# Optimization experiments

Measured on AMD Instinct MI355X. Metric: run time of the kernel, lower is better.

## Reference

```python
import jax, jax.numpy as jnp
import numpy as np

HEADS = 16

def setup_inputs() -> dict:
    key = jax.random.key(0)
    k1, k2, k3, k4 = jax.random.split(key, 4)
    B, T, S, W = 2, 2048, 2048, 1024
    x = jax.random.normal(k1, (B, T, W), dtype=jnp.float32)
    cond_k = jax.random.normal(k2, (B, S, W), dtype=jnp.float32)
    cond_v = jax.random.normal(k3, (B, S, W), dtype=jnp.float32)
    w_proj = jax.random.normal(k4, (W, W), dtype=jnp.float32) * 0.02
    b_proj = jnp.zeros((W,), dtype=jnp.float32)
    return {"x": x, "cond_k": cond_k, "cond_v": cond_v, "w_proj": w_proj, "b_proj": b_proj}

def reference(x, cond_k, cond_v, w_proj, b_proj):
    B, T, W = x.shape
    S = cond_k.shape[1]
    H = HEADS
    d = W // H
    scale = 1.0 / jnp.sqrt(jnp.sqrt(jnp.float32(d)))  # applied to both q and k
    q = x.reshape(B, T, H, d) * scale
    k = cond_k.reshape(B, S, H, d) * scale
    v = cond_v.reshape(B, S, H, d)
    # scores: [B, H, T, S]
    scores = jnp.einsum('bthd,bshd->bhts', q, k)
    w = jax.nn.softmax(scores.astype(jnp.float32), axis=-1).astype(scores.dtype)
    out = jnp.einsum('bhts,bshd->bthd', w, v).reshape(B, T, W)
    # c_proj: torch Linear -> x @ W.T + b
    return out @ w_proj.T + b_proj
```

## Files before the change

kernel.cpp:

```cpp
#include <hip/hip_runtime.h>

#define Bn 2
#define Hn 16
#define Tn 2048
#define Sn 2048
#define Wd 1024
#define Dh 64

typedef __attribute__((ext_vector_type(8))) short s16x8;
typedef __attribute__((ext_vector_type(4))) short s16x4;
typedef __attribute__((ext_vector_type(4))) float f32x4;

#define MFMA(a, b, c) __builtin_amdgcn_mfma_f32_16x16x32_bf16((a), (b), (c), 0, 0, 0)

__device__ __forceinline__ s16x8 ld8(const short* p) { return *(const s16x8*)p; }

__device__ __forceinline__ short f2bf(float f) {
    unsigned u = __builtin_bit_cast(unsigned, f);
    u += 0x7FFFu + ((u >> 16) & 1u);
    return (short)(u >> 16);
}

__global__ void cvt_scale(const float* __restrict__ in, short* __restrict__ out,
                          int n, float s) {
    int i = (blockIdx.x * 256 + threadIdx.x) * 8;
    if (i < n) {
        float4 a = *(const float4*)(in + i);
        float4 b = *(const float4*)(in + i + 4);
        s16x8 o;
        o[0] = f2bf(a.x * s); o[1] = f2bf(a.y * s); o[2] = f2bf(a.z * s); o[3] = f2bf(a.w * s);
        o[4] = f2bf(b.x * s); o[5] = f2bf(b.y * s); o[6] = f2bf(b.z * s); o[7] = f2bf(b.w * s);
        *(s16x8*)(out + i) = o;
    }
}

__global__ __launch_bounds__(256) void vtrans(const float* __restrict__ cv,
                                              short* __restrict__ vt) {
    __shared__ short T[64][68];
    const int st = blockIdx.x & 31;
    const int bh = blockIdx.x >> 5;
    const int b = bh >> 4, h = bh & 15;
    const int tid = threadIdx.x;
#pragma unroll
    for (int i = 0; i < 4; ++i) {
        int f = i * 256 + tid, sr = f >> 4, c4 = f & 15;
        float4 v = *(const float4*)(cv + (size_t)(b * Sn + st * 64 + sr) * Wd + h * Dh + c4 * 4);
        s16x4 o;
        o[0] = f2bf(v.x); o[1] = f2bf(v.y); o[2] = f2bf(v.z); o[3] = f2bf(v.w);
        *(s16x4*)&T[sr][c4 * 4] = o;
    }
    __syncthreads();
#pragma unroll
    for (int i = 0; i < 4; ++i) {
        int f = i * 256 + tid, dr = f >> 4, p4 = f & 15;
        s16x4 o;
#pragma unroll
        for (int k = 0; k < 4; ++k) {
            int p = p4 * 4 + k;
            int g = p >> 5, pi = p & 31;
            int sl = g * 32 + ((pi & 1) * 16 + (pi >> 1));
            o[k] = T[sl][dr];
        }
        *(s16x4*)(vt + (size_t)(bh * Dh + dr) * Sn + st * 64 + p4 * 4) = o;
    }
}

#define KSTR 72

__global__ __launch_bounds__(256, 2) void attn_fused(
    const float* __restrict__ x, const short* __restrict__ kb,
    const short* __restrict__ vt, short* __restrict__ ao)
{
    __shared__ short Ks[64 * KSTR];
    __shared__ short Vs[64 * KSTR];
    __shared__ short Pt[4][32 * KSTR];

    const int tid  = threadIdx.x;
    const int w    = tid >> 6;
    const int l    = tid & 63;
    const int quad = l >> 4;
    const int l16  = l & 15;

    const int bh = blockIdx.x & 31;
    const int qt = blockIdx.x >> 5;
    const int b  = bh >> 4, h = bh & 15;

    const int qrow0 = qt * 128 + w * 32;

    const float SQ = 0.125f * 1.4426950408889634f;
    s16x8 aq[2][2];
#pragma unroll
    for (int mi = 0; mi < 2; ++mi)
#pragma unroll
        for (int c = 0; c < 2; ++c) {
            const float* p = x + (size_t)(b * Tn + qrow0 + mi * 16 + l16) * Wd
                               + h * Dh + c * 32 + quad * 8;
            float4 a = ((const float4*)p)[0], bb = ((const float4*)p)[1];
            s16x8 o;
            o[0] = f2bf(a.x * SQ); o[1] = f2bf(a.y * SQ); o[2] = f2bf(a.z * SQ); o[3] = f2bf(a.w * SQ);
            o[4] = f2bf(bb.x * SQ); o[5] = f2bf(bb.y * SQ); o[6] = f2bf(bb.z * SQ); o[7] = f2bf(bb.w * SQ);
            aq[mi][c] = o;
        }

    f32x4 oacc[2][4];
    float dn[2][4];
#pragma unroll
    for (int mi = 0; mi < 2; ++mi) {
#pragma unroll
        for (int nt = 0; nt < 4; ++nt) {
            oacc[mi][nt][0] = 0.f; oacc[mi][nt][1] = 0.f;
            oacc[mi][nt][2] = 0.f; oacc[mi][nt][3] = 0.f;
        }
#pragma unroll
        for (int r = 0; r < 4; ++r) dn[mi][r] = 0.f;
    }

    const short* kb_h = kb + (size_t)(b * Sn) * Wd + h * Dh;
    const short* vt_h = vt + (size_t)(bh * Dh) * Sn;

    const int sr = tid >> 3;
    const int sg = tid & 7;

    short* Pw = &Pt[w][0];

    for (int it = 0; it < Sn / 64; ++it) {
        const int s0 = it * 64;
        __syncthreads();
#pragma unroll
        for (int i = 0; i < 2; ++i) {
            int r0 = sr + i * 32;
            *(s16x8*)&Ks[r0 * KSTR + sg * 8] = ld8(kb_h + (size_t)(s0 + r0) * Wd + sg * 8);
            *(s16x8*)&Vs[r0 * KSTR + sg * 8] = ld8(vt_h + (size_t)r0 * Sn + s0 + sg * 8);
        }
        __syncthreads();

        f32x4 sc[2][4];
        const f32x4 z = {0.f, 0.f, 0.f, 0.f};
#pragma unroll
        for (int sj = 0; sj < 4; ++sj) {
            s16x8 k0 = *(const s16x8*)&Ks[(sj * 16 + l16) * KSTR + quad * 8];
            s16x8 k1 = *(const s16x8*)&Ks[(sj * 16 + l16) * KSTR + 32 + quad * 8];
#pragma unroll
            for (int mi = 0; mi < 2; ++mi) {
                sc[mi][sj] = MFMA(aq[mi][0], k0, z);
                sc[mi][sj] = MFMA(aq[mi][1], k1, sc[mi][sj]);
            }
        }

#pragma unroll
        for (int mi = 0; mi < 2; ++mi)
#pragma unroll
            for (int g = 0; g < 2; ++g)
#pragma unroll
                for (int r = 0; r < 4; ++r) {
                    unsigned u0 = __builtin_bit_cast(unsigned, __builtin_amdgcn_exp2f(sc[mi][2 * g][r]));
                    unsigned u1 = __builtin_bit_cast(unsigned, __builtin_amdgcn_exp2f(sc[mi][2 * g + 1][r]));
                    unsigned hi = u1 & 0xFFFF0000u;
                    unsigned pk = (u0 >> 16) | hi;
                    dn[mi][r] += __builtin_bit_cast(float, u0 & 0xFFFF0000u)
                               + __builtin_bit_cast(float, hi);
                    *(unsigned*)&Pw[(mi * 16 + quad * 4 + r) * KSTR + g * 32 + l16 * 2] = pk;
                }
        __asm__ __volatile__("" ::: "memory");

        s16x8 ap[2][2], bv[4][2];
#pragma unroll
        for (int mi = 0; mi < 2; ++mi)
#pragma unroll
            for (int g = 0; g < 2; ++g)
                ap[mi][g] = *(const s16x8*)&Pw[(mi * 16 + l16) * KSTR + g * 32 + quad * 8];
#pragma unroll
        for (int nt = 0; nt < 4; ++nt)
#pragma unroll
            for (int g = 0; g < 2; ++g)
                bv[nt][g] = *(const s16x8*)&Vs[(nt * 16 + l16) * KSTR + g * 32 + quad * 8];
#pragma unroll
        for (int mi = 0; mi < 2; ++mi)
#pragma unroll
            for (int nt = 0; nt < 4; ++nt) {
                oacc[mi][nt] = MFMA(ap[mi][0], bv[nt][0], oacc[mi][nt]);
                oacc[mi][nt] = MFMA(ap[mi][1], bv[nt][1], oacc[mi][nt]);
            }
    }

#pragma unroll
    for (int mi = 0; mi < 2; ++mi)
#pragma unroll
        for (int r = 0; r < 4; ++r) {
            float d = dn[mi][r];
            d += __shfl_xor(d, 1);
            d += __shfl_xor(d, 2);
            d += __shfl_xor(d, 4);
            d += __shfl_xor(d, 8);
            float inv = 1.0f / d;
            int t = qrow0 + mi * 16 + quad * 4 + r;
#pragma unroll
            for (int nt = 0; nt < 4; ++nt)
                ao[(size_t)(b * Tn + t) * Wd + h * Dh + nt * 16 + l16] =
                    f2bf(oacc[mi][nt][r] * inv);
        }
}

#define LSTR 40

__global__ __launch_bounds__(256, 2) void proj_gemm(
    const short* __restrict__ A, const short* __restrict__ Wb,
    const float* __restrict__ bias, float* __restrict__ out)
{
    __shared__ short As[128 * LSTR];
    __shared__ short Bs[64 * LSTR];

    const int tid  = threadIdx.x;
    const int w    = tid >> 6;
    const int l    = tid & 63;
    const int quad = l >> 4;
    const int l16  = l & 15;

    const int bn = blockIdx.x & 15;
    const int bm = blockIdx.x >> 4;
    const int m0 = bm * 128;
    const int n0 = bn * 64;
    const int wm = (w & 1) * 64;
    const int wn = (w >> 1) * 32;

    const int rr = tid >> 2;
    const int sg = tid & 3;

    f32x4 acc[4][2];
#pragma unroll
    for (int mi = 0; mi < 4; ++mi)
#pragma unroll
        for (int nt = 0; nt < 2; ++nt) {
            acc[mi][nt][0] = 0.f; acc[mi][nt][1] = 0.f;
            acc[mi][nt][2] = 0.f; acc[mi][nt][3] = 0.f;
        }

    for (int k0 = 0; k0 < Wd; k0 += 32) {
        __syncthreads();
        *(s16x8*)&As[rr * LSTR + sg * 8]        = ld8(A  + (size_t)(m0 + rr) * Wd + k0 + sg * 8);
        *(s16x8*)&As[(rr + 64) * LSTR + sg * 8] = ld8(A  + (size_t)(m0 + 64 + rr) * Wd + k0 + sg * 8);
        *(s16x8*)&Bs[rr * LSTR + sg * 8]        = ld8(Wb + (size_t)(n0 + rr) * Wd + k0 + sg * 8);
        __syncthreads();

        s16x8 a[4], bw[2];
#pragma unroll
        for (int mi = 0; mi < 4; ++mi)
            a[mi] = *(const s16x8*)&As[(wm + mi * 16 + l16) * LSTR + quad * 8];
#pragma unroll
        for (int nt = 0; nt < 2; ++nt)
            bw[nt] = *(const s16x8*)&Bs[(wn + nt * 16 + l16) * LSTR + quad * 8];
#pragma unroll
        for (int mi = 0; mi < 4; ++mi)
#pragma unroll
            for (int nt = 0; nt < 2; ++nt)
                acc[mi][nt] = MFMA(a[mi], bw[nt], acc[mi][nt]);
    }

#pragma unroll
    for (int nt = 0; nt < 2; ++nt) {
        float bv = bias[n0 + wn + nt * 16 + l16];
#pragma unroll
        for (int mi = 0; mi < 4; ++mi)
#pragma unroll
            for (int r = 0; r < 4; ++r)
                out[(size_t)(m0 + wm + mi * 16 + quad * 4 + r) * Wd + n0 + wn + nt * 16 + l16] =
                    acc[mi][nt][r] + bv;
    }
}

extern "C" void kernel_launch(void* const* d_in, const int* in_sizes, int n_in,
                              void* d_out, int out_size, void* d_ws, size_t ws_size,
                              hipStream_t stream) {
    const float* x  = (const float*)d_in[0];
    const float* ck = (const float*)d_in[1];
    const float* cv = (const float*)d_in[2];
    const float* wp = (const float*)d_in[3];
    const float* bp = (const float*)d_in[4];

    const int nX = Bn * Tn * Wd;
    const int nW = Wd * Wd;

    short* kbb = (short*)d_ws;
    short* vtb = kbb + nX;
    short* wbb = vtb + nX;
    short* am  = wbb + nW;

    cvt_scale<<<dim3(nX / 2048), dim3(256), 0, stream>>>(ck, kbb, nX, 1.0f);
    cvt_scale<<<dim3(nW / 2048), dim3(256), 0, stream>>>(wp, wbb, nW, 1.0f);
    vtrans<<<dim3(1024), dim3(256), 0, stream>>>(cv, vtb);

    attn_fused<<<dim3(Bn * Hn * (Tn / 128)), dim3(256), 0, stream>>>(x, kbb, vtb, am);
    proj_gemm<<<dim3((Bn * Tn / 128) * (Wd / 64)), dim3(256), 0, stream>>>(
        am, wbb, bp, (float*)d_out);
}
```

Before: 179.0 us.

## Double-buffer K/V and GEMM tiles with register prefetch, vectorize P stores

The attention and projection kernels now prefetch the next K/V (or A/W) tile into registers while computing on the current LDS buffer, then write it to the alternate buffer. This cuts one barrier per iteration and overlaps global-load latency with MFMA work. The V transpose permutation is changed so that P can be written as 64-bit packed stores, and s_setprio is raised around the MFMA blocks. The cost is doubled LDS use and extra registers, which could reduce occupancy.

Result: faster. 168.4 us (-6.0%).

```diff
diff --git a/kernel.cpp b/kernel.cpp
--- a/kernel.cpp
+++ b/kernel.cpp
@@ -10,6 +10,7 @@
 typedef __attribute__((ext_vector_type(8))) short s16x8;
 typedef __attribute__((ext_vector_type(4))) short s16x4;
 typedef __attribute__((ext_vector_type(4))) float f32x4;
+typedef __attribute__((ext_vector_type(2))) unsigned u32x2;
 
 #define MFMA(a, b, c) __builtin_amdgcn_mfma_f32_16x16x32_bf16((a), (b), (c), 0, 0, 0)
 
@@ -56,10 +57,7 @@
         s16x4 o;
 #pragma unroll
         for (int k = 0; k < 4; ++k) {
-            int p = p4 * 4 + k;
-            int g = p >> 5, pi = p & 31;
-            int sl = g * 32 + ((pi & 1) * 16 + (pi >> 1));
-            o[k] = T[sl][dr];
+            o[k] = T[k * 16 + p4][dr];
         }
         *(s16x4*)(vt + (size_t)(bh * Dh + dr) * Sn + st * 64 + p4 * 4) = o;
     }
@@ -71,9 +69,9 @@
     const float* __restrict__ x, const short* __restrict__ kb,
     const short* __restrict__ vt, short* __restrict__ ao)
 {
-    __shared__ short Ks[64 * KSTR];
-    __shared__ short Vs[64 * KSTR];
-    __shared__ short Pt[4][32 * KSTR];
+    __shared__ alignas(16) short Ks[2][64 * KSTR];
+    __shared__ alignas(16) short Vs[2][64 * KSTR];
+    __shared__ alignas(16) short Pt[4][32 * KSTR];
 
     const int tid  = threadIdx.x;
     const int w    = tid >> 6;
@@ -123,44 +121,70 @@
 
     short* Pw = &Pt[w][0];
 
-    for (int it = 0; it < Sn / 64; ++it) {
-        const int s0 = it * 64;
-        __syncthreads();
-#pragma unroll
-        for (int i = 0; i < 2; ++i) {
-            int r0 = sr + i * 32;
-            *(s16x8*)&Ks[r0 * KSTR + sg * 8] = ld8(kb_h + (size_t)(s0 + r0) * Wd + sg * 8);
-            *(s16x8*)&Vs[r0 * KSTR + sg * 8] = ld8(vt_h + (size_t)r0 * Sn + s0 + sg * 8);
-        }
-        __syncthreads();
+    s16x8 kr[2], vr[2];
+#pragma unroll
+    for (int i = 0; i < 2; ++i) {
+        int r0 = sr + i * 32;
+        kr[i] = ld8(kb_h + (size_t)r0 * Wd + sg * 8);
+        vr[i] = ld8(vt_h + (size_t)r0 * Sn + sg * 8);
+    }
+#pragma unroll
+    for (int i = 0; i < 2; ++i) {
+        int r0 = sr + i * 32;
+        *(s16x8*)&Ks[0][r0 * KSTR + sg * 8] = kr[i];
+        *(s16x8*)&Vs[0][r0 * KSTR + sg * 8] = vr[i];
+    }
+    __syncthreads();
+
+    const int NIT = Sn / 64;
+    for (int it = 0; it < NIT; ++it) {
+        const int p = it & 1;
+
+        if (it + 1 < NIT) {
+            const int s1 = (it + 1) * 64;
+#pragma unroll
+            for (int i = 0; i < 2; ++i) {
+                int r0 = sr + i * 32;
+                kr[i] = ld8(kb_h + (size_t)(s1 + r0) * Wd + sg * 8);
+                vr[i] = ld8(vt_h + (size_t)r0 * Sn + s1 + sg * 8);
+            }
+        }
 
         f32x4 sc[2][4];
         const f32x4 z = {0.f, 0.f, 0.f, 0.f};
+        __builtin_amdgcn_s_setprio(1);
 #pragma unroll
         for (int sj = 0; sj < 4; ++sj) {
-            s16x8 k0 = *(const s16x8*)&Ks[(sj * 16 + l16) * KSTR + quad * 8];
-            s16x8 k1 = *(const s16x8*)&Ks[(sj * 16 + l16) * KSTR + 32 + quad * 8];
+            s16x8 k0 = *(const s16x8*)&Ks[p][(sj * 16 + l16) * KSTR + quad * 8];
+            s16x8 k1 = *(const s16x8*)&Ks[p][(sj * 16 + l16) * KSTR + 32 + quad * 8];
 #pragma unroll
             for (int mi = 0; mi < 2; ++mi) {
                 sc[mi][sj] = MFMA(aq[mi][0], k0, z);
                 sc[mi][sj] = MFMA(aq[mi][1], k1, sc[mi][sj]);
             }
         }
+        __builtin_amdgcn_s_setprio(0);
 
 #pragma unroll
         for (int mi = 0; mi < 2; ++mi)
 #pragma unroll
-            for (int g = 0; g < 2; ++g)
-#pragma unroll
-                for (int r = 0; r < 4; ++r) {
-                    unsigned u0 = __builtin_bit_cast(unsigned, __builtin_amdgcn_exp2f(sc[mi][2 * g][r]));
-                    unsigned u1 = __builtin_bit_cast(unsigned, __builtin_amdgcn_exp2f(sc[mi][2 * g + 1][r]));
-                    unsigned hi = u1 & 0xFFFF0000u;
-                    unsigned pk = (u0 >> 16) | hi;
-                    dn[mi][r] += __builtin_bit_cast(float, u0 & 0xFFFF0000u)
-                               + __builtin_bit_cast(float, hi);
-                    *(unsigned*)&Pw[(mi * 16 + quad * 4 + r) * KSTR + g * 32 + l16 * 2] = pk;
-                }
+            for (int r = 0; r < 4; ++r) {
+                unsigned u0 = __builtin_bit_cast(unsigned, __builtin_amdgcn_exp2f(sc[mi][0][r]));
+                unsigned u1 = __builtin_bit_cast(unsigned, __builtin_amdgcn_exp2f(sc[mi][1][r]));
+                unsigned u2 = __builtin_bit_cast(unsigned, __builtin_amdgcn_exp2f(sc[mi][2][r]));
+                unsigned u3 = __builtin_bit_cast(unsigned, __builtin_amdgcn_exp2f(sc[mi][3][r]));
+                unsigned h1 = u1 & 0xFFFF0000u;
+                unsigned h3 = u3 & 0xFFFF0000u;
+                unsigned w0 = (u0 >> 16) | h1;
+                unsigned w1 = (u2 >> 16) | h3;
+                float t0 = __builtin_bit_cast(float, u0 & 0xFFFF0000u)
+                         + __builtin_bit_cast(float, h1);
+                float t1 = __builtin_bit_cast(float, u2 & 0xFFFF0000u)
+                         + __builtin_bit_cast(float, h3);
+                dn[mi][r] += t0 + t1;
+                u32x2 pk; pk[0] = w0; pk[1] = w1;
+                *(u32x2*)&Pw[(mi * 16 + quad * 4 + r) * KSTR + l16 * 4] = pk;
+            }
         __asm__ __volatile__("" ::: "memory");
 
         s16x8 ap[2][2], bv[4][2];
@@ -173,7 +197,8 @@
         for (int nt = 0; nt < 4; ++nt)
 #pragma unroll
             for (int g = 0; g < 2; ++g)
-                bv[nt][g] = *(const s16x8*)&Vs[(nt * 16 + l16) * KSTR + g * 32 + quad * 8];
+                bv[nt][g] = *(const s16x8*)&Vs[p][(nt * 16 + l16) * KSTR + g * 32 + quad * 8];
+        __builtin_amdgcn_s_setprio(1);
 #pragma unroll
         for (int mi = 0; mi < 2; ++mi)
 #pragma unroll
@@ -181,6 +206,17 @@
                 oacc[mi][nt] = MFMA(ap[mi][0], bv[nt][0], oacc[mi][nt]);
                 oacc[mi][nt] = MFMA(ap[mi][1], bv[nt][1], oacc[mi][nt]);
             }
+        __builtin_amdgcn_s_setprio(0);
+
+        if (it + 1 < NIT) {
+#pragma unroll
+            for (int i = 0; i < 2; ++i) {
+                int r0 = sr + i * 32;
+                *(s16x8*)&Ks[p ^ 1][r0 * KSTR + sg * 8] = kr[i];
+                *(s16x8*)&Vs[p ^ 1][r0 * KSTR + sg * 8] = vr[i];
+            }
+        }
+        __syncthreads();
     }
 
 #pragma unroll
@@ -207,8 +243,8 @@
     const short* __restrict__ A, const short* __restrict__ Wb,
     const float* __restrict__ bias, float* __restrict__ out)
 {
-    __shared__ short As[128 * LSTR];
-    __shared__ short Bs[64 * LSTR];
+    __shared__ alignas(16) short As[2][128 * LSTR];
+    __shared__ alignas(16) short Bs[2][64 * LSTR];
 
     const int tid  = threadIdx.x;
     const int w    = tid >> 6;
@@ -235,25 +271,44 @@
             acc[mi][nt][2] = 0.f; acc[mi][nt][3] = 0.f;
         }
 
+    s16x8 ra0 = ld8(A  + (size_t)(m0 + rr) * Wd + sg * 8);
+    s16x8 ra1 = ld8(A  + (size_t)(m0 + 64 + rr) * Wd + sg * 8);
+    s16x8 rb  = ld8(Wb + (size_t)(n0 + rr) * Wd + sg * 8);
+    *(s16x8*)&As[0][rr * LSTR + sg * 8]        = ra0;
+    *(s16x8*)&As[0][(rr + 64) * LSTR + sg * 8] = ra1;
+    *(s16x8*)&Bs[0][rr * LSTR + sg * 8]        = rb;
+    __syncthreads();
+
     for (int k0 = 0; k0 < Wd; k0 += 32) {
-        __syncthreads();
-        *(s16x8*)&As[rr * LSTR + sg * 8]        = ld8(A  + (size_t)(m0 + rr) * Wd + k0 + sg * 8);
-        *(s16x8*)&As[(rr + 64) * LSTR + sg * 8] = ld8(A  + (size_t)(m0 + 64 + rr) * Wd + k0 + sg * 8);
-        *(s16x8*)&Bs[rr * LSTR + sg * 8]        = ld8(Wb + (size_t)(n0 + rr) * Wd + k0 + sg * 8);
-        __syncthreads();
+        const int p = (k0 >> 5) & 1;
+
+        if (k0 + 32 < Wd) {
+            ra0 = ld8(A  + (size_t)(m0 + rr) * Wd + k0 + 32 + sg * 8);
+            ra1 = ld8(A  + (size_t)(m0 + 64 + rr) * Wd + k0 + 32 + sg * 8);
+            rb  = ld8(Wb + (size_t)(n0 + rr) * Wd + k0 + 32 + sg * 8);
+        }
 
         s16x8 a[4], bw[2];
 #pragma unroll
         for (int mi = 0; mi < 4; ++mi)
-            a[mi] = *(const s16x8*)&As[(wm + mi * 16 + l16) * LSTR + quad * 8];
+            a[mi] = *(const s16x8*)&As[p][(wm + mi * 16 + l16) * LSTR + quad * 8];
 #pragma unroll
         for (int nt = 0; nt < 2; ++nt)
-            bw[nt] = *(const s16x8*)&Bs[(wn + nt * 16 + l16) * LSTR + quad * 8];
+            bw[nt] = *(const s16x8*)&Bs[p][(wn + nt * 16 + l16) * LSTR + quad * 8];
+        __builtin_amdgcn_s_setprio(1);
 #pragma unroll
         for (int mi = 0; mi < 4; ++mi)
 #pragma unroll
             for (int nt = 0; nt < 2; ++nt)
                 acc[mi][nt] = MFMA(a[mi], bw[nt], acc[mi][nt]);
+        __builtin_amdgcn_s_setprio(0);
+
+        if (k0 + 32 < Wd) {
+            *(s16x8*)&As[p ^ 1][rr * LSTR + sg * 8]        = ra0;
+            *(s16x8*)&As[p ^ 1][(rr + 64) * LSTR + sg * 8] = ra1;
+            *(s16x8*)&Bs[p ^ 1][rr * LSTR + sg * 8]        = rb;
+        }
+        __syncthreads();
     }
 
 #pragma unroll
```
